# Kernel optimization log

Measured on AMD Instinct MI355X. Metric: run time of the kernel, lower is better.

The kernel has to match this reference:

```python
import jax, jax.numpy as jnp
import numpy as np


def _rigid_matrix(p1, p2, w):
    # p1, p2: [B, N, 3]; w: [B, 1, N] (weights summing to 1 over N)
    p1 = jnp.swapaxes(p1, 1, 2)  # [B,3,N]
    p2 = jnp.swapaxes(p2, 1, 2)
    p1_c = jnp.sum(p1 * w, axis=2, keepdims=True)  # weighted centroid [B,3,1]
    p2_c = jnp.sum(p2 * w, axis=2, keepdims=True)
    q1 = (p1 - p1_c) * w
    q2 = (p2 - p2_c) * w
    Hm = jnp.einsum('bin,bjn->bij', q1, q2)  # [B,3,3] cross-covariance
    U, _, Vt = jnp.linalg.svd(Hm, full_matrices=False)
    V = jnp.swapaxes(Vt, 1, 2)
    Ut = jnp.swapaxes(U, 1, 2)
    R = V @ Ut
    det = jnp.linalg.det(R)  # [B]
    s = jnp.sign(det)
    # original scales the third ROW of V by sign(det) (rows [1,1,sign])
    scale = jnp.stack([jnp.ones_like(s), jnp.ones_like(s), s], axis=1)[:, :, None]  # [B,3,1]
    V = V * scale
    R = V @ Ut
    T = p2_c - R @ p1_c  # [B,3,1]
    return jnp.concatenate([R, T], axis=-1)  # [B,3,4]


def _affine_grid_3d(theta, D, H, W):
    # matches torch F.affine_grid(theta, (B,C,D,H,W), align_corners=False)
    def coords(n):
        return (2.0 * jnp.arange(n, dtype=theta.dtype) + 1.0) / n - 1.0
    zs, ys, xs = coords(D), coords(H), coords(W)
    Z, Y, X = jnp.meshgrid(zs, ys, xs, indexing='ij')
    base = jnp.stack([X, Y, Z], axis=-1)  # [D,H,W,3], last dim = (x,y,z)
    grid = jnp.einsum('dhwj,bij->bdhwi', base, theta[:, :, :3])
    grid = grid + theta[:, None, None, None, :, 3]
    return grid  # [B,D,H,W,3]


def setup_inputs() -> dict:
    key = jax.random.key(0)
    k1, k2, k3 = jax.random.split(key, 3)
    B, N = 4, 128
    points_m = jax.random.normal(k1, (B, N, 3), jnp.float32) * 0.5
    points_f = jax.random.normal(k2, (B, N, 3), jnp.float32) * 0.5
    w = jax.random.uniform(k3, (B, 1, N), jnp.float32)
    weights = w / jnp.sum(w, axis=-1, keepdims=True)  # normalized -> valid centroid weights
    return {"points_m": points_m, "points_f": points_f, "weights": weights,
            "D": 160, "H": 192, "W": 160}


def reference(points_m, points_f, weights, D, H, W):
    # forward = grid_from_points: matrix = get_matrix(points_f, points_m, w)
    theta = _rigid_matrix(points_f, points_m, weights)
    return _affine_grid_3d(theta, D, H, W)
```

## Files before the change

### kernel.cpp

```cpp
#include <hip/hip_runtime.h>
#include <math.h>

#define B_ 4
#define N_ 128
#define D_ 160
#define H_ 192
#define W_ 160

typedef float floatx4 __attribute__((ext_vector_type(4)));

__global__ __launch_bounds__(256) void rigid_kernel(const float* __restrict__ pm,
                                                    const float* __restrict__ pf,
                                                    const float* __restrict__ wt,
                                                    float* __restrict__ theta) {
  __shared__ float bc[B_][15];
  const int tid = threadIdx.x;
  const int b = tid >> 6;
  const int lane = tid & 63;

  const int base = b * N_;
  float wA = wt[base + lane], wB = wt[base + lane + 64];
  float fA[3], fB[3], mA[3], mB[3];
#pragma unroll
  for (int c = 0; c < 3; ++c) {
    fA[c] = pf[(base + lane) * 3 + c];
    fB[c] = pf[(base + lane + 64) * 3 + c];
    mA[c] = pm[(base + lane) * 3 + c];
    mB[c] = pm[(base + lane + 64) * 3 + c];
  }

  float sums[6];
#pragma unroll
  for (int c = 0; c < 3; ++c) {
    sums[c]     = wA * fA[c] + wB * fB[c];
    sums[3 + c] = wA * mA[c] + wB * mB[c];
  }
#pragma unroll
  for (int k = 0; k < 6; ++k) {
    float v = sums[k];
#pragma unroll
    for (int o = 1; o < 64; o <<= 1) v += __shfl_xor(v, o, 64);
    sums[k] = v;
  }

  float q1A[3], q1B[3], q2A[3], q2B[3];
#pragma unroll
  for (int c = 0; c < 3; ++c) {
    q1A[c] = (fA[c] - sums[c]) * wA;     q1B[c] = (fB[c] - sums[c]) * wB;
    q2A[c] = (mA[c] - sums[3 + c]) * wA; q2B[c] = (mB[c] - sums[3 + c]) * wB;
  }
  float Hm[9];
#pragma unroll
  for (int i = 0; i < 3; ++i)
#pragma unroll
    for (int j = 0; j < 3; ++j)
      Hm[i * 3 + j] = q1A[i] * q2A[j] + q1B[i] * q2B[j];
#pragma unroll
  for (int k = 0; k < 9; ++k) {
    float v = Hm[k];
#pragma unroll
    for (int o = 1; o < 64; o <<= 1) v += __shfl_xor(v, o, 64);
    Hm[k] = v;
  }

  if (lane == 0) {
#pragma unroll
    for (int k = 0; k < 6; ++k) bc[b][k] = sums[k];
#pragma unroll
    for (int k = 0; k < 9; ++k) bc[b][6 + k] = Hm[k];
  }
  __syncthreads();

  if (tid < B_) {
    const int bb = tid;
    float X[3][3];
    float fr = 0.0f;
#pragma unroll
    for (int i = 0; i < 3; ++i)
#pragma unroll
      for (int j = 0; j < 3; ++j) {
        X[i][j] = bc[bb][6 + i * 3 + j];
        fr = fmaf(X[i][j], X[i][j], fr);
      }
    fr = sqrtf(fr);
    if (fr < 1e-30f) fr = 1.0f;
    const float ifr = 1.0f / fr;
#pragma unroll
    for (int i = 0; i < 3; ++i)
#pragma unroll
      for (int j = 0; j < 3; ++j) X[i][j] *= ifr;

    for (int it = 0; it < 8; ++it) {
      float C[3][3];
      C[0][0] =  X[1][1] * X[2][2] - X[1][2] * X[2][1];
      C[0][1] = -(X[1][0] * X[2][2] - X[1][2] * X[2][0]);
      C[0][2] =  X[1][0] * X[2][1] - X[1][1] * X[2][0];
      C[1][0] = -(X[0][1] * X[2][2] - X[0][2] * X[2][1]);
      C[1][1] =  X[0][0] * X[2][2] - X[0][2] * X[2][0];
      C[1][2] = -(X[0][0] * X[2][1] - X[0][1] * X[2][0]);
      C[2][0] =  X[0][1] * X[1][2] - X[0][2] * X[1][1];
      C[2][1] = -(X[0][0] * X[1][2] - X[0][2] * X[1][0]);
      C[2][2] =  X[0][0] * X[1][1] - X[0][1] * X[1][0];
      float det = X[0][0] * C[0][0] + X[0][1] * C[0][1] + X[0][2] * C[0][2];
      float ad = fabsf(det);
      float mu = (ad > 1e-30f && ad < 1e30f)
                     ? exp2f(log2f(ad) * (-1.0f / 3.0f)) : 1.0f;
      float inv = 1.0f / (mu * det);
#pragma unroll
      for (int i = 0; i < 3; ++i)
#pragma unroll
        for (int j = 0; j < 3; ++j)
          X[i][j] = 0.5f * fmaf(mu, X[i][j], C[i][j] * inv);
    }

    float R[3][3];
#pragma unroll
    for (int i = 0; i < 3; ++i)
#pragma unroll
      for (int j = 0; j < 3; ++j) R[i][j] = X[j][i];

    float det = R[0][0] * (R[1][1] * R[2][2] - R[1][2] * R[2][1])
              - R[0][1] * (R[1][0] * R[2][2] - R[1][2] * R[2][0])
              + R[0][2] * (R[1][0] * R[2][1] - R[1][1] * R[2][0]);
    float s = (det < 0.0f) ? -1.0f : 1.0f;
    R[2][0] *= s; R[2][1] *= s; R[2][2] *= s;

    const float c1d[3] = {bc[bb][0], bc[bb][1], bc[bb][2]};
    const float c2d[3] = {bc[bb][3], bc[bb][4], bc[bb][5]};
#pragma unroll
    for (int i = 0; i < 3; ++i) {
      float Ti = c2d[i] - (R[i][0] * c1d[0] + R[i][1] * c1d[1] + R[i][2] * c1d[2]);
      theta[bb * 12 + i * 4 + 0] = R[i][0];
      theta[bb * 12 + i * 4 + 1] = R[i][1];
      theta[bb * 12 + i * 4 + 2] = R[i][2];
      theta[bb * 12 + i * 4 + 3] = Ti;
    }
  }
}

#define F_PER_ROW ((W_ * 3) / 4)
#define F4_TOTAL (B_ * D_ * H_ * F_PER_ROW)
#define BLOCKS_PER_BATCH 1800

__global__ __launch_bounds__(256) void grid_kernel(const float* __restrict__ theta,
                                                   floatx4* __restrict__ out) {
  const int tid = threadIdx.x;
  const int blk = blockIdx.x;
  const int b = blk / BLOCKS_PER_BATCH;

  const float* th = theta + b * 12;
  const float r00 = th[0], r01 = th[1], r02 = th[2],  t0 = th[3];
  const float r10 = th[4], r11 = th[5], r12 = th[6],  t1 = th[7];
  const float r20 = th[8], r21 = th[9], r22 = th[10], t2 = th[11];
  const float dx = 2.0f / (float)W_;

  int f = blk * 2048 + tid;
#pragma unroll
  for (int k = 0; k < 8; ++k, f += 256) {
    const int row = f / F_PER_ROW;
    const int lf4 = f - row * F_PER_ROW;
    const int h = row % H_;
    const int d = (row / H_) % D_;

    const int lf = lf4 * 4;
    const int w0 = lf / 3;
    const int phase = lf - 3 * w0;

    const float y = (2.0f * (float)h + 1.0f) * (1.0f / (float)H_) - 1.0f;
    const float z = (2.0f * (float)d + 1.0f) * (1.0f / (float)D_) - 1.0f;
    const float x0 = (2.0f * (float)w0 + 1.0f) * (1.0f / (float)W_) - 1.0f;

    const float A0 = fmaf(r00, x0, fmaf(r01, y, fmaf(r02, z, t0)));
    const float A1 = fmaf(r10, x0, fmaf(r11, y, fmaf(r12, z, t1)));
    const float A2 = fmaf(r20, x0, fmaf(r21, y, fmaf(r22, z, t2)));
    const float B0 = fmaf(r00, dx, A0);
    const float B1 = fmaf(r10, dx, A1);
    const float B2 = fmaf(r20, dx, A2);

    floatx4 o;
    o.x = (phase == 0) ? A0 : ((phase == 1) ? A1 : A2);
    o.y = (phase == 0) ? A1 : ((phase == 1) ? A2 : B0);
    o.z = (phase == 0) ? A2 : ((phase == 1) ? B0 : B1);
    o.w = (phase == 0) ? B0 : ((phase == 1) ? B1 : B2);

    out[f] = o;
  }
}

extern "C" void kernel_launch(void* const* d_in, const int* in_sizes, int n_in,
                              void* d_out, int out_size, void* d_ws, size_t ws_size,
                              hipStream_t stream) {
  const float* pm = (const float*)d_in[0];
  const float* pf = (const float*)d_in[1];
  const float* wt = (const float*)d_in[2];
  float* theta = (float*)d_ws;
  floatx4* out = (floatx4*)d_out;

  rigid_kernel<<<1, 256, 0, stream>>>(pm, pf, wt, theta);

  const int nBlocks = F4_TOTAL / 2048;
  grid_kernel<<<nBlocks, 256, 0, stream>>>(theta, out);
}
```

Baseline: 44.61 us.

## Fuse rigid-matrix solve into grid kernel with per-block redundant computation

```diff
diff --git a/kernel.cpp b/kernel.cpp
--- a/kernel.cpp
+++ b/kernel.cpp
@@ -9,17 +9,23 @@
 
 typedef float floatx4 __attribute__((ext_vector_type(4)));
 
-__global__ __launch_bounds__(256) void rigid_kernel(const float* __restrict__ pm,
+#define F_PER_ROW ((W_ * 3) / 4)
+#define F4_TOTAL (B_ * D_ * H_ * F_PER_ROW)
+#define NBLOCKS 1800
+#define F4_PER_BLOCK (F4_TOTAL / NBLOCKS)
+#define BLOCKS_PER_BATCH (NBLOCKS / B_)
+
+__global__ __launch_bounds__(256) void fused_kernel(const float* __restrict__ pm,
                                                     const float* __restrict__ pf,
                                                     const float* __restrict__ wt,
-                                                    float* __restrict__ theta) {
-  __shared__ float bc[B_][15];
+                                                    floatx4* __restrict__ out) {
   const int tid = threadIdx.x;
-  const int b = tid >> 6;
+  const int blk = blockIdx.x;
+  const int b = blk / BLOCKS_PER_BATCH;
   const int lane = tid & 63;
 
   const int base = b * N_;
-  float wA = wt[base + lane], wB = wt[base + lane + 64];
+  const float wA = wt[base + lane], wB = wt[base + lane + 64];
   float fA[3], fB[3], mA[3], mB[3];
 #pragma unroll
   for (int c = 0; c < 3; ++c) {
@@ -49,39 +55,28 @@
     q1A[c] = (fA[c] - sums[c]) * wA;     q1B[c] = (fB[c] - sums[c]) * wB;
     q2A[c] = (mA[c] - sums[3 + c]) * wA; q2B[c] = (mB[c] - sums[3 + c]) * wB;
   }
-  float Hm[9];
+  float X[3][3];
 #pragma unroll
   for (int i = 0; i < 3; ++i)
 #pragma unroll
     for (int j = 0; j < 3; ++j)
-      Hm[i * 3 + j] = q1A[i] * q2A[j] + q1B[i] * q2B[j];
+      X[i][j] = q1A[i] * q2A[j] + q1B[i] * q2B[j];
 #pragma unroll
-  for (int k = 0; k < 9; ++k) {
-    float v = Hm[k];
+  for (int i = 0; i < 3; ++i)
 #pragma unroll
-    for (int o = 1; o < 64; o <<= 1) v += __shfl_xor(v, o, 64);
-    Hm[k] = v;
-  }
+    for (int j = 0; j < 3; ++j) {
+      float v = X[i][j];
+#pragma unroll
+      for (int o = 1; o < 64; o <<= 1) v += __shfl_xor(v, o, 64);
+      X[i][j] = v;
+    }
 
-  if (lane == 0) {
-#pragma unroll
-    for (int k = 0; k < 6; ++k) bc[b][k] = sums[k];
-#pragma unroll
-    for (int k = 0; k < 9; ++k) bc[b][6 + k] = Hm[k];
-  }
-  __syncthreads();
-
-  if (tid < B_) {
-    const int bb = tid;
-    float X[3][3];
+  {
     float fr = 0.0f;
 #pragma unroll
     for (int i = 0; i < 3; ++i)
 #pragma unroll
-      for (int j = 0; j < 3; ++j) {
-        X[i][j] = bc[bb][6 + i * 3 + j];
-        fr = fmaf(X[i][j], X[i][j], fr);
-      }
+      for (int j = 0; j < 3; ++j) fr = fmaf(X[i][j], X[i][j], fr);
     fr = sqrtf(fr);
     if (fr < 1e-30f) fr = 1.0f;
     const float ifr = 1.0f / fr;
@@ -89,74 +84,54 @@
     for (int i = 0; i < 3; ++i)
 #pragma unroll
       for (int j = 0; j < 3; ++j) X[i][j] *= ifr;
+  }
 
-    for (int it = 0; it < 8; ++it) {
-      float C[3][3];
-      C[0][0] =  X[1][1] * X[2][2] - X[1][2] * X[2][1];
-      C[0][1] = -(X[1][0] * X[2][2] - X[1][2] * X[2][0]);
-      C[0][2] =  X[1][0] * X[2][1] - X[1][1] * X[2][0];
-      C[1][0] = -(X[0][1] * X[2][2] - X[0][2] * X[2][1]);
-      C[1][1] =  X[0][0] * X[2][2] - X[0][2] * X[2][0];
-      C[1][2] = -(X[0][0] * X[2][1] - X[0][1] * X[2][0]);
-      C[2][0] =  X[0][1] * X[1][2] - X[0][2] * X[1][1];
-      C[2][1] = -(X[0][0] * X[1][2] - X[0][2] * X[1][0]);
-      C[2][2] =  X[0][0] * X[1][1] - X[0][1] * X[1][0];
-      float det = X[0][0] * C[0][0] + X[0][1] * C[0][1] + X[0][2] * C[0][2];
-      float ad = fabsf(det);
-      float mu = (ad > 1e-30f && ad < 1e30f)
-                     ? exp2f(log2f(ad) * (-1.0f / 3.0f)) : 1.0f;
-      float inv = 1.0f / (mu * det);
-#pragma unroll
-      for (int i = 0; i < 3; ++i)
-#pragma unroll
-        for (int j = 0; j < 3; ++j)
-          X[i][j] = 0.5f * fmaf(mu, X[i][j], C[i][j] * inv);
-    }
-
-    float R[3][3];
+  for (int it = 0; it < 8; ++it) {
+    float C[3][3];
+    C[0][0] =  X[1][1] * X[2][2] - X[1][2] * X[2][1];
+    C[0][1] = -(X[1][0] * X[2][2] - X[1][2] * X[2][0]);
+    C[0][2] =  X[1][0] * X[2][1] - X[1][1] * X[2][0];
+    C[1][0] = -(X[0][1] * X[2][2] - X[0][2] * X[2][1]);
+    C[1][1] =  X[0][0] * X[2][2] - X[0][2] * X[2][0];
+    C[1][2] = -(X[0][0] * X[2][1] - X[0][1] * X[2][0]);
+    C[2][0] =  X[0][1] * X[1][2] - X[0][2] * X[1][1];
+    C[2][1] = -(X[0][0] * X[1][2] - X[0][2] * X[1][0]);
+    C[2][2] =  X[0][0] * X[1][1] - X[0][1] * X[1][0];
+    float det = X[0][0] * C[0][0] + X[0][1] * C[0][1] + X[0][2] * C[0][2];
+    float ad = fabsf(det);
+    float mu = (ad > 1e-30f && ad < 1e30f)
+                   ? exp2f(log2f(ad) * (-1.0f / 3.0f)) : 1.0f;
+    float inv = 1.0f / (mu * det);
 #pragma unroll
     for (int i = 0; i < 3; ++i)
 #pragma unroll
-      for (int j = 0; j < 3; ++j) R[i][j] = X[j][i];
+      for (int j = 0; j < 3; ++j)
+        X[i][j] = 0.5f * fmaf(mu, X[i][j], C[i][j] * inv);
+  }
 
+  float R[3][3];
+#pragma unroll
+  for (int i = 0; i < 3; ++i)
+#pragma unroll
+    for (int j = 0; j < 3; ++j) R[i][j] = X[j][i];
+  {
     float det = R[0][0] * (R[1][1] * R[2][2] - R[1][2] * R[2][1])
               - R[0][1] * (R[1][0] * R[2][2] - R[1][2] * R[2][0])
               + R[0][2] * (R[1][0] * R[2][1] - R[1][1] * R[2][0]);
     float s = (det < 0.0f) ? -1.0f : 1.0f;
     R[2][0] *= s; R[2][1] *= s; R[2][2] *= s;
-
-    const float c1d[3] = {bc[bb][0], bc[bb][1], bc[bb][2]};
-    const float c2d[3] = {bc[bb][3], bc[bb][4], bc[bb][5]};
-#pragma unroll
-    for (int i = 0; i < 3; ++i) {
-      float Ti = c2d[i] - (R[i][0] * c1d[0] + R[i][1] * c1d[1] + R[i][2] * c1d[2]);
-      theta[bb * 12 + i * 4 + 0] = R[i][0];
-      theta[bb * 12 + i * 4 + 1] = R[i][1];
-      theta[bb * 12 + i * 4 + 2] = R[i][2];
-      theta[bb * 12 + i * 4 + 3] = Ti;
-    }
   }
-}
-
-#define F_PER_ROW ((W_ * 3) / 4)
-#define F4_TOTAL (B_ * D_ * H_ * F_PER_ROW)
-#define BLOCKS_PER_BATCH 1800
-
-__global__ __launch_bounds__(256) void grid_kernel(const float* __restrict__ theta,
-                                                   floatx4* __restrict__ out) {
-  const int tid = threadIdx.x;
-  const int blk = blockIdx.x;
-  const int b = blk / BLOCKS_PER_BATCH;
-
-  const float* th = theta + b * 12;
-  const float r00 = th[0], r01 = th[1], r02 = th[2],  t0 = th[3];
-  const float r10 = th[4], r11 = th[5], r12 = th[6],  t1 = th[7];
-  const float r20 = th[8], r21 = th[9], r22 = th[10], t2 = th[11];
+  const float t0 = sums[3] - (R[0][0] * sums[0] + R[0][1] * sums[1] + R[0][2] * sums[2]);
+  const float t1 = sums[4] - (R[1][0] * sums[0] + R[1][1] * sums[1] + R[1][2] * sums[2]);
+  const float t2 = sums[5] - (R[2][0] * sums[0] + R[2][1] * sums[1] + R[2][2] * sums[2]);
+  const float r00 = R[0][0], r01 = R[0][1], r02 = R[0][2];
+  const float r10 = R[1][0], r11 = R[1][1], r12 = R[1][2];
+  const float r20 = R[2][0], r21 = R[2][1], r22 = R[2][2];
   const float dx = 2.0f / (float)W_;
 
-  int f = blk * 2048 + tid;
-#pragma unroll
-  for (int k = 0; k < 8; ++k, f += 256) {
+  int f = blk * F4_PER_BLOCK + tid;
+#pragma unroll 4
+  for (int k = 0; k < 32; ++k, f += 256) {
     const int row = f / F_PER_ROW;
     const int lf4 = f - row * F_PER_ROW;
     const int h = row % H_;
@@ -193,11 +168,7 @@
   const float* pm = (const float*)d_in[0];
   const float* pf = (const float*)d_in[1];
   const float* wt = (const float*)d_in[2];
-  float* theta = (float*)d_ws;
   floatx4* out = (floatx4*)d_out;
 
-  rigid_kernel<<<1, 256, 0, stream>>>(pm, pf, wt, theta);
-
-  const int nBlocks = F4_TOTAL / 2048;
-  grid_kernel<<<nBlocks, 256, 0, stream>>>(theta, out);
+  fused_kernel<<<NBLOCKS, 256, 0, stream>>>(pm, pf, wt, out);
 }
```

Result: slower. 51.30 us (+15.0%).
